# Optimization experiments

Hardware: AMD Instinct MI355X
Metric: run time of the kernel (lower is better)

The kernel has to match this reference:

```python
import math
import jax, jax.numpy as jnp
import numpy as np

NUM_PRE_NMS = 2000
NMS_THR = 0.7
MIN_SIZE = 16.0
LOG_MAX = math.log(1000.0 / 16)  # clamp on dh, dw as in the torch module

B, A, H, W = 8, 3, 200, 304
STRIDE = 4


def _make_anchors():
    # grid anchors, channel-last anchor ordering to match permute(0,2,3,1)
    sizes = np.array([32.0, 64.0, 128.0], dtype=np.float32)  # A sizes
    ys = (np.arange(H, dtype=np.float32) + 0.5) * STRIDE
    xs = (np.arange(W, dtype=np.float32) + 0.5) * STRIDE
    cy, cx = np.meshgrid(ys, xs, indexing="ij")  # [H,W]
    cx = cx[:, :, None]
    cy = cy[:, :, None]
    half = (sizes / 2.0)[None, None, :]  # [1,1,A]
    anc = np.stack([cx - half, cy - half, cx + half, cy + half], axis=-1)  # [H,W,A,4]
    anc = anc.reshape(-1, 4)  # [H*W*A, 4]
    anc = np.broadcast_to(anc[None], (B, anc.shape[0], 4)).copy()
    return jnp.asarray(anc)


def setup_inputs() -> dict:
    key = jax.random.key(0)
    k1, k2 = jax.random.split(key)
    cls_logits = jax.random.normal(k1, (B, A, H, W), dtype=jnp.float32)
    regs = jax.random.normal(k2, (B, 4 * A, H, W), dtype=jnp.float32) * 0.1
    anchors = _make_anchors()
    return {"cls_logits": cls_logits, "regs": regs, "anchors": anchors,
            "image_h": 800, "image_w": 1216}


def _box_iou(boxes):
    # boxes: [K,4] -> iou [K,K]
    x1, y1, x2, y2 = boxes[:, 0], boxes[:, 1], boxes[:, 2], boxes[:, 3]
    area = (x2 - x1) * (y2 - y1)
    ix1 = jnp.maximum(x1[:, None], x1[None, :])
    iy1 = jnp.maximum(y1[:, None], y1[None, :])
    ix2 = jnp.minimum(x2[:, None], x2[None, :])
    iy2 = jnp.minimum(y2[:, None], y2[None, :])
    iw = jnp.clip(ix2 - ix1, 0.0)
    ih = jnp.clip(iy2 - iy1, 0.0)
    inter = iw * ih
    union = area[:, None] + area[None, :] - inter
    return inter / jnp.maximum(union, 1e-6)


def _nms_one(boxes, valid):
    # boxes sorted by descending score; greedy suppression, fixed-size keep mask
    k = boxes.shape[0]
    iou = _box_iou(boxes)
    later = jnp.arange(k)

    def body(i, keep):
        sup = (iou[i] > NMS_THR) & keep[i] & (later > i)
        return keep & ~sup

    return jax.lax.fori_loop(0, k, body, valid)


def reference(cls_logits, regs, anchors, image_h, image_w):
    b = cls_logits.shape[0]
    # scores/regs in channel-last anchor order (matches permute(0,2,3,1))
    scores = jnp.transpose(cls_logits, (0, 2, 3, 1)).reshape(b, -1)       # [B,N]
    deltas = jnp.transpose(regs, (0, 2, 3, 1)).reshape(b, -1, 4)          # [B,N,4]
    n = scores.shape[1]
    k = min(NUM_PRE_NMS, n)

    top_scores, idx = jax.lax.top_k(scores, k)                            # [B,K]
    top_deltas = jnp.take_along_axis(deltas, idx[:, :, None], axis=1)     # [B,K,4]
    top_anchors = jnp.take_along_axis(anchors, idx[:, :, None], axis=1)   # [B,K,4]

    dx, dy = top_deltas[..., 0], top_deltas[..., 1]
    dh = jnp.minimum(top_deltas[..., 2], LOG_MAX)
    dw = jnp.minimum(top_deltas[..., 3], LOG_MAX)
    ah = top_anchors[..., 3] - top_anchors[..., 1]
    aw = top_anchors[..., 2] - top_anchors[..., 0]
    cx = aw / 2
    cy = ah / 2
    px = cx + dx * aw
    py = cy + dy * ah
    ph = jnp.exp(dh) * ah
    pw = jnp.exp(dw) * aw
    boxes = jnp.stack([px - pw / 2, py - ph / 2, px + pw / 2, py + ph / 2], axis=-1)  # [B,K,4]

    # size filter on clamped coords (as in _nms)
    w_img = jnp.float32(image_w)
    h_img = jnp.float32(image_h)
    bw = jnp.clip(boxes[..., 2], 0.0, w_img) - jnp.clip(boxes[..., 0], 0.0, w_img)
    bh = jnp.clip(boxes[..., 3], 0.0, h_img) - jnp.clip(boxes[..., 1], 0.0, h_img)
    valid = (bw >= MIN_SIZE) & (bh >= MIN_SIZE)

    keep = jax.vmap(_nms_one)(boxes, valid)                               # [B,K]
    out_boxes = boxes * keep[..., None].astype(boxes.dtype)
    return out_boxes, top_scores, keep
```

## Files before the change

kernel.cpp:

```cpp
#include <hip/hip_runtime.h>

#define HWSZ 60800
#define NA 3
#define NTOT 182400
#define KSEL 2000
#define CANDCAP 8192
#define SELCAP 4096
#define NBATCH 8
#define GSPLIT 128
#define LOG_MAX_F 4.135166556742356f

#define OFF_H1    0
#define OFF_CCNT  65536
#define OFF_SCNT  65568
#define ZR_BYTES  65600
#define OFF_SEL   65600
#define OFF_BOX   65728
#define OFF_VALID 321728
#define OFF_SUP   385728
#define OFF_CAND  385728
#define OFF_SELK  910016

__device__ __forceinline__ unsigned int xform(float f) {
    unsigned int b = __float_as_uint(f);
    return b ^ ((unsigned int)((int)b >> 31) | 0x80000000u);
}

__global__ __launch_bounds__(256) void k_hist1(const float* __restrict__ cls,
                                               unsigned int* __restrict__ hist1) {
    int b = blockIdx.y, part = blockIdx.x, tid = threadIdx.x;
    __shared__ unsigned int h[2048];
    for (int i = tid; i < 2048; i += 256) h[i] = 0u;
    __syncthreads();
    const float4* base4 = (const float4*)(cls + (size_t)b * NTOT);
    const int n4 = NTOT / 4;
    int per = (n4 + GSPLIT - 1) / GSPLIT;
    int lo = part * per, hi = lo + per;
    if (hi > n4) hi = n4;
    for (int i = lo + tid; i < hi; i += 256) {
        float4 v = base4[i];
        atomicAdd(&h[xform(v.x) >> 21], 1u);
        atomicAdd(&h[xform(v.y) >> 21], 1u);
        atomicAdd(&h[xform(v.z) >> 21], 1u);
        atomicAdd(&h[xform(v.w) >> 21], 1u);
    }
    __syncthreads();
    unsigned int* gh = hist1 + b * 2048;
    for (int i = tid; i < 2048; i += 256)
        if (h[i]) atomicAdd(&gh[i], h[i]);
}

__global__ __launch_bounds__(1024) void k_scan1(const unsigned int* __restrict__ hist1,
                                                uint4* __restrict__ selinfo) {
    int b = blockIdx.x, tid = threadIdx.x;
    __shared__ unsigned int sa[2048], sb[2048];
    const unsigned int* h = hist1 + b * 2048;
    sa[tid] = h[tid];
    sa[tid + 1024] = h[tid + 1024];
    unsigned int* src = sa; unsigned int* dst = sb;
    for (int d = 1; d < 2048; d <<= 1) {
        __syncthreads();
        dst[tid] = src[tid] + ((tid + d < 2048) ? src[tid + d] : 0u);
        int i2 = tid + 1024;
        dst[i2] = src[i2] + ((i2 + d < 2048) ? src[i2 + d] : 0u);
        unsigned int* t = src; src = dst; dst = t;
    }
    __syncthreads();
    #pragma unroll
    for (int k = 0; k < 2; ++k) {
        int i = tid + k * 1024;
        unsigned int c = src[i];
        unsigned int cn = (i < 2047) ? src[i + 1] : 0u;
        if (c >= KSEL && cn < KSEL)
            selinfo[b] = make_uint4((unsigned int)i, cn, KSEL - cn, 0u);
    }
}

__global__ __launch_bounds__(256) void k_gather(const float* __restrict__ cls,
                                                const uint4* __restrict__ selinfo,
                                                unsigned long long* __restrict__ cand,
                                                unsigned int* __restrict__ ccnt) {
    int b = blockIdx.y, part = blockIdx.x, tid = threadIdx.x;
    unsigned int bin = selinfo[b].x;
    __shared__ unsigned long long lbuf[1024];
    __shared__ unsigned int lcnt, gbase;
    if (tid == 0) lcnt = 0u;
    __syncthreads();
    const float4* base4 = (const float4*)(cls + (size_t)b * NTOT);
    const int n4 = NTOT / 4;
    int per = (n4 + GSPLIT - 1) / GSPLIT;
    int lo = part * per, hi = lo + per;
    if (hi > n4) hi = n4;
    for (int i = lo + tid; i < hi; i += 256) {
        float4 v = base4[i];
        float vals[4] = {v.x, v.y, v.z, v.w};
        int idx0 = i * 4;
        #pragma unroll
        for (int q = 0; q < 4; ++q) {
            unsigned int u = xform(vals[q]);
            if ((u >> 21) >= bin) {
                int idx = idx0 + q;
                int a = idx / HWSZ;
                int hw = idx - a * HWSZ;
                unsigned int n = (unsigned int)(hw * NA + a);
                unsigned int pos = atomicAdd(&lcnt, 1u);
                if (pos < 1024u)
                    lbuf[pos] = ((unsigned long long)u << 32) | (unsigned long long)(~n);
            }
        }
    }
    __syncthreads();
    if (tid == 0) {
        unsigned int c = lcnt < 1024u ? lcnt : 1024u;
        gbase = atomicAdd(&ccnt[b], c);
    }
    __syncthreads();
    unsigned int c = lcnt < 1024u ? lcnt : 1024u;
    unsigned int gb = gbase;
    for (unsigned int i = tid; i < c; i += 256) {
        unsigned int p = gb + i;
        if (p < CANDCAP) cand[(size_t)b * CANDCAP + p] = lbuf[i];
    }
}

__global__ __launch_bounds__(1024) void k_refine(const unsigned long long* __restrict__ cand,
                                                 const unsigned int* __restrict__ ccnt,
                                                 const uint4* __restrict__ selinfo,
                                                 unsigned long long* __restrict__ selk,
                                                 unsigned int* __restrict__ scnt) {
    int b = blockIdx.x;
    int tid = threadIdx.x;
    __shared__ unsigned int sa[2048], sb[2048];
    __shared__ unsigned int acnt, shT;
    uint4 si = selinfo[b];
    unsigned int bin = si.x, krem = si.z;
    unsigned int m = ccnt[b];
    if (m > CANDCAP) m = CANDCAP;
    const unsigned long long* cb = cand + (size_t)b * CANDCAP;

    sa[tid] = 0u; sa[tid + 1024] = 0u;
    if (tid == 0) acnt = 0u;
    __syncthreads();
    for (unsigned int i = tid; i < m; i += 1024) {
        unsigned int u = (unsigned int)(cb[i] >> 32);
        if ((u >> 21) == bin) atomicAdd(&sa[(u >> 10) & 2047u], 1u);
    }
    unsigned int* src = sa; unsigned int* dst = sb;
    for (int d = 1; d < 2048; d <<= 1) {
        __syncthreads();
        dst[tid] = src[tid] + ((tid + d < 2048) ? src[tid + d] : 0u);
        int i2 = tid + 1024;
        dst[i2] = src[i2] + ((i2 + d < 2048) ? src[i2 + d] : 0u);
        unsigned int* t = src; src = dst; dst = t;
    }
    __syncthreads();
    #pragma unroll
    for (int k = 0; k < 2; ++k) {
        int i = tid + k * 1024;
        unsigned int c = src[i];
        unsigned int cn = (i < 2047) ? src[i + 1] : 0u;
        if (c >= krem && cn < krem)
            shT = (bin << 21) | ((unsigned int)i << 10);
    }
    __syncthreads();
    unsigned int T = shT;

    int lane = tid & 63;
    unsigned long long lmask = (1ULL << lane) - 1ULL;
    unsigned int mr = (m + 1023u) & ~1023u;
    unsigned long long* sout = selk + (size_t)b * SELCAP;
    for (unsigned int i = tid; i < mr; i += 1024) {
        bool pred = false;
        unsigned long long key = 0ULL;
        if (i < m) {
            key = cb[i];
            pred = ((unsigned int)(key >> 32)) >= T;
        }
        unsigned long long mask = __ballot(pred);
        unsigned int cw = (unsigned int)__popcll(mask);
        unsigned int base = 0u;
        if (lane == 0 && cw) base = atomicAdd(&acnt, cw);
        base = __shfl(base, 0, 64);
        if (pred) {
            unsigned int pos = base + (unsigned int)__popcll(mask & lmask);
            if (pos < SELCAP) sout[pos] = key;
        }
    }
    __syncthreads();
    if (tid == 0) scnt[b] = (acnt < SELCAP) ? acnt : SELCAP;
}

__global__ __launch_bounds__(256) void k_rank_decode(
        const unsigned long long* __restrict__ selk,
        const unsigned int* __restrict__ scnt,
        const float* __restrict__ regs,
        const float* __restrict__ anchors,
        const int* __restrict__ img_h,
        const int* __restrict__ img_w,
        float* __restrict__ out_scores,
        float4* __restrict__ boxes_ws,
        unsigned int* __restrict__ valid_ws) {
    int b = blockIdx.y;
    int tid = threadIdx.x;
    unsigned int sc = scnt[b];
    if (sc > SELCAP) sc = SELCAP;
    unsigned int kbase = blockIdx.x * 64;
    if (kbase >= sc) return;
    int ki = tid & 63;
    int q = tid >> 6;
    int lane = tid & 63;
    const unsigned long long* sb_ = selk + (size_t)b * SELCAP;
    unsigned int r = kbase + (unsigned int)ki;
    unsigned long long mykey = (r < sc) ? sb_[r] : 0ULL;

    unsigned int qs = ((sc + 255u) >> 8) << 6;
    unsigned int lo = (unsigned int)q * qs;
    unsigned int hi = lo + qs;
    if (hi > sc) hi = sc;

    unsigned int cnt = 0u;
    for (unsigned int base = lo; base < hi; base += 64) {
        unsigned long long kj = 0ULL;
        if (base + (unsigned int)lane < hi) kj = sb_[base + lane];
        unsigned int klo = (unsigned int)kj;
        unsigned int khi = (unsigned int)(kj >> 32);
        #pragma unroll
        for (int t = 0; t < 64; ++t) {
            unsigned int lo_ = (unsigned int)__builtin_amdgcn_readlane((int)klo, t);
            unsigned int hi_ = (unsigned int)__builtin_amdgcn_readlane((int)khi, t);
            unsigned long long kt = ((unsigned long long)hi_ << 32) | (unsigned long long)lo_;
            cnt += (kt > mykey) ? 1u : 0u;
        }
    }
    __shared__ unsigned int cntsh[4][64];
    cntsh[q][ki] = cnt;
    __syncthreads();
    if (tid >= 64) return;
    unsigned int rank = cntsh[0][ki] + cntsh[1][ki] + cntsh[2][ki] + cntsh[3][ki];
    if (r >= sc || rank >= KSEL) return;

    int hv = img_h[0];
    int wv = img_w[0];
    float himg = (hv > 0 && hv < 100000) ? (float)hv : __int_as_float(hv);
    float wimg = (wv > 0 && wv < 100000) ? (float)wv : __int_as_float(wv);

    unsigned int u = (unsigned int)(mykey >> 32);
    unsigned int n = ~((unsigned int)mykey);
    unsigned int bits = (u & 0x80000000u) ? (u & 0x7FFFFFFFu) : ~u;
    float score = __uint_as_float(bits);
    int a = (int)(n % NA);
    int hw = (int)(n / NA);
    const float* rp = regs + ((size_t)b * (4 * NA) + 4 * a) * HWSZ + hw;
    float dx = rp[0 * HWSZ];
    float dy = rp[1 * HWSZ];
    float dh = rp[2 * HWSZ];
    float dw = rp[3 * HWSZ];
    const float* ap = anchors + ((size_t)b * NTOT + n) * 4;
    float ax1 = ap[0], ay1 = ap[1], ax2 = ap[2], ay2 = ap[3];
    float ahh = ay2 - ay1;
    float aww = ax2 - ax1;
    float cx = aww * 0.5f;
    float cy = ahh * 0.5f;
    float px = cx + dx * aww;
    float py = cy + dy * ahh;
    dh = fminf(dh, LOG_MAX_F);
    dw = fminf(dw, LOG_MAX_F);
    float ph = expf(dh) * ahh;
    float pw = expf(dw) * aww;
    float x1 = px - pw * 0.5f;
    float y1 = py - ph * 0.5f;
    float x2 = px + pw * 0.5f;
    float y2 = py + ph * 0.5f;
    float bwv = fminf(fmaxf(x2, 0.f), wimg) - fminf(fmaxf(x1, 0.f), wimg);
    float bhv = fminf(fmaxf(y2, 0.f), himg) - fminf(fmaxf(y1, 0.f), himg);
    unsigned int valid = (bwv >= 16.f && bhv >= 16.f) ? 1u : 0u;
    size_t o = (size_t)b * KSEL + rank;
    out_scores[o] = score;
    boxes_ws[o] = make_float4(x1, y1, x2, y2);
    valid_ws[o] = valid;
}

__global__ __launch_bounds__(256) void k_supmat(const float4* __restrict__ boxes_ws,
                                                unsigned long long* __restrict__ sup) {
    int ct = blockIdx.x;
    int rt = blockIdx.y;
    int b  = blockIdx.z;
    int tid = threadIdx.x;
    __shared__ float4 colbox[64];
    int j0 = ct * 64;
    if (tid < 64) {
        int jl = j0 + tid;
        colbox[tid] = (jl < KSEL) ? boxes_ws[(size_t)b * KSEL + jl]
                                  : make_float4(0.f, 0.f, 0.f, 0.f);
    }
    __syncthreads();
    int i = rt * 256 + tid;
    if (i >= KSEL) return;
    float4 bi = boxes_ws[(size_t)b * KSEL + i];
    float area_i = (bi.z - bi.x) * (bi.w - bi.y);
    unsigned long long word = 0ULL;
    #pragma unroll 8
    for (int jj = 0; jj < 64; ++jj) {
        int j = j0 + jj;
        float4 bj = colbox[jj];
        float area_j = (bj.z - bj.x) * (bj.w - bj.y);
        float ix1 = fmaxf(bi.x, bj.x);
        float iy1 = fmaxf(bi.y, bj.y);
        float ix2 = fminf(bi.z, bj.z);
        float iy2 = fminf(bi.w, bj.w);
        float iw = fmaxf(ix2 - ix1, 0.f);
        float ih = fmaxf(iy2 - iy1, 0.f);
        float inter = iw * ih;
        float uni = area_i + area_j - inter;
        float iou = inter / fmaxf(uni, 1e-6f);
        bool s = (j > i) && (j < KSEL) && (iou > 0.7f);
        if (s) word |= (1ULL << jj);
    }
    sup[((size_t)b * KSEL + i) * 32 + ct] = word;
}

#define LOAD_TILE(wnext, buf)                                                \
    {                                                                        \
        int gbase_ = (wnext) * 2048;                                         \
        _Pragma("unroll")                                                    \
        for (int k = 0; k < 8; ++k) {                                        \
            int e_ = tid + k * 256;                                          \
            int row_ = (wnext) * 64 + (e_ >> 5);                             \
            buf[k] = (row_ < KSEL) ? srow[gbase_ + e_] : 0ULL;               \
        }                                                                    \
    }

#define PROCESS_TILE(w, buf)                                                 \
    {                                                                        \
        if (myword == (w)) {                                                 \
            _Pragma("unroll")                                                \
            for (int k = 0; k < 8; ++k)                                      \
                diag[(tid >> 5) + k * 8] = buf[k];                           \
        }                                                                    \
        __syncthreads();      \
        unsigned long long dval_ = diag[lane];                               \
        unsigned long long nz_ = __ballot(dval_ != 0ULL);                    \
        unsigned int dlo_ = (unsigned int)dval_;                             \
        unsigned int dhi_ = (unsigned int)(dval_ >> 32);                     \
        unsigned long long pend_ =                                           \
            ((unsigned long long)accw[(w) * 2 + 1] << 32)                    \
            | (unsigned long long)accw[(w) * 2];                             \
        unsigned long long c64_ = kws[w] & ~pend_;                           \
        unsigned int clo_ = __builtin_amdgcn_readfirstlane((unsigned int)c64_);        \
        unsigned int chi_ = __builtin_amdgcn_readfirstlane((unsigned int)(c64_ >> 32));\
        unsigned long long cur_ = ((unsigned long long)chi_ << 32)           \
                                  | (unsigned long long)clo_;                \
        if (cur_) {                                                          \
             \
            unsigned long long rem_ = cur_ & nz_;                            \
            while (rem_) {                                                   \
                int bit_ = __builtin_ctzll(rem_);                            \
                unsigned int lo_ = (unsigned int)__builtin_amdgcn_readlane((int)dlo_, bit_); \
                unsigned int hi_ = (unsigned int)__builtin_amdgcn_readlane((int)dhi_, bit_); \
                unsigned long long d_ = ((unsigned long long)hi_ << 32)      \
                                        | (unsigned long long)lo_;           \
                cur_ &= ~d_;                                                 \
                rem_ = cur_ & nz_ & ~((2ULL << bit_) - 1ULL);                \
            }                                                                \
            if (tid == 0) fin[w] = cur_;                                     \
            unsigned long long v_ = 0ULL;                                    \
            _Pragma("unroll")                                                \
            for (int k = 0; k < 8; ++k) {                                    \
                int row_ = (tid >> 5) + k * 8;                               \
                if ((cur_ >> row_) & 1ULL) v_ |= buf[k];                     \
            }                                                                \
            v_ |= __shfl_xor(v_, 32, 64);                                    \
            if (lane < 32 && v_) {                                           \
                atomicOr(&accw[myword * 2], (unsigned int)v_);               \
                atomicOr(&accw[myword * 2 + 1], (unsigned int)(v_ >> 32));   \
            }                                                                \
        } else if (tid == 0) {                                               \
            fin[w] = 0ULL;                                                   \
        }                                                                    \
    }

__global__ __launch_bounds__(256) void k_nms_scan(const unsigned long long* __restrict__ sup,
                                                  const unsigned int* __restrict__ valid_ws,
                                                  const float4* __restrict__ boxes_ws,
                                                  float* __restrict__ out_boxes,
                                                  float* __restrict__ out_keep) {
    int b = blockIdx.x;
    int tid = threadIdx.x;
    int lane = tid & 63;
    int myword = tid & 31;
    __shared__ unsigned long long kws[32];
    __shared__ unsigned long long fin[32];
    __shared__ unsigned long long diag[64];
    __shared__ unsigned int accw[64];
    const unsigned long long* srow = sup + (size_t)b * KSEL * 32;

    if (tid < 32) {
        unsigned long long kw = 0ULL;
        const uint4* vv = (const uint4*)(valid_ws + (size_t)b * KSEL);
        #pragma unroll 4
        for (int q = 0; q < 16; ++q) {
            uint4 x = vv[tid * 16 + q];
            int base = q * 4;
            if (x.x) kw |= 1ULL << (base + 0);
            if (x.y) kw |= 1ULL << (base + 1);
            if (x.z) kw |= 1ULL << (base + 2);
            if (x.w) kw |= 1ULL << (base + 3);
        }
        if (tid == 31) kw &= 0xFFFFULL;
        kws[tid] = kw;
    }
    if (tid < 64) accw[tid] = 0u;

    unsigned long long A[8], B[8];
    LOAD_TILE(0, A);
    LOAD_TILE(1, B);

    for (int t = 0; t < 16; ++t) {
        int w = 2 * t;
        PROCESS_TILE(w, A);
        if (w + 2 < 32) LOAD_TILE(w + 2, A);
        PROCESS_TILE(w + 1, B);
        if (w + 3 < 32) LOAD_TILE(w + 3, B);
    }
    __syncthreads();

    for (int r = tid; r < KSEL; r += 256) {
        float kf = (float)((fin[r >> 6] >> (r & 63)) & 1ULL);
        size_t o = (size_t)b * KSEL + r;
        out_keep[o] = kf;
        float4 bx = boxes_ws[o];
        float* ob = out_boxes + o * 4;
        ob[0] = bx.x * kf;
        ob[1] = bx.y * kf;
        ob[2] = bx.z * kf;
        ob[3] = bx.w * kf;
    }
}

extern "C" void kernel_launch(void* const* d_in, const int* in_sizes, int n_in,
                              void* d_out, int out_size, void* d_ws, size_t ws_size,
                              hipStream_t stream) {
    const float* cls     = (const float*)d_in[0];
    const float* regs    = (const float*)d_in[1];
    const float* anchors = (const float*)d_in[2];
    const int*   img_h   = (const int*)d_in[3];
    const int*   img_w   = (const int*)d_in[4];

    float* out = (float*)d_out;
    float* out_boxes  = out;
    float* out_scores = out + 64000;
    float* out_keep   = out + 80000;

    char* ws = (char*)d_ws;
    unsigned int* hist1      = (unsigned int*)(ws + OFF_H1);
    unsigned int* ccnt       = (unsigned int*)(ws + OFF_CCNT);
    unsigned int* scnt       = (unsigned int*)(ws + OFF_SCNT);
    uint4* selinfo           = (uint4*)(ws + OFF_SEL);
    float4* boxes_ws         = (float4*)(ws + OFF_BOX);
    unsigned int* valid_ws   = (unsigned int*)(ws + OFF_VALID);
    unsigned long long* sup  = (unsigned long long*)(ws + OFF_SUP);
    unsigned long long* cand = (unsigned long long*)(ws + OFF_CAND);
    unsigned long long* selk = (unsigned long long*)(ws + OFF_SELK);

    hipMemsetAsync(ws, 0, ZR_BYTES, stream);
    k_hist1<<<dim3(GSPLIT, NBATCH), 256, 0, stream>>>(cls, hist1);
    k_scan1<<<NBATCH, 1024, 0, stream>>>(hist1, selinfo);
    k_gather<<<dim3(GSPLIT, NBATCH), 256, 0, stream>>>(cls, selinfo, cand, ccnt);
    k_refine<<<NBATCH, 1024, 0, stream>>>(cand, ccnt, selinfo, selk, scnt);
    k_rank_decode<<<dim3(SELCAP / 64, NBATCH), 256, 0, stream>>>(selk, scnt, regs, anchors,
                                                                 img_h, img_w, out_scores,
                                                                 boxes_ws, valid_ws);
    k_supmat<<<dim3(32, 8, NBATCH), 256, 0, stream>>>(boxes_ws, sup);
    k_nms_scan<<<NBATCH, 256, 0, stream>>>(sup, valid_ws, boxes_ws, out_boxes, out_keep);
}
```

Measured before the change: 200.7 us.

## Fuse histogram scan into last block, drop refine pass, skip lower-triangle suppression tiles

The histogram kernel now runs the prefix scan itself: an atomic done-counter picks the last block per batch, which removes a separate launch. The refine kernel is deleted, so rank_decode ranks every gathered candidate directly (up to CANDCAP), with its grid widened to match. The suppression-matrix kernel skips tiles that lie entirely below the diagonal, NMS accumulation ignores words that are already final, and box output is written as float4. These changes cut launches and redundant work, but ranking now covers a larger candidate set and its cost grows quadratically with it.

After: 244.6 us. +21.9%, slower.

```diff
diff --git a/kernel.cpp b/kernel.cpp
--- a/kernel.cpp
+++ b/kernel.cpp
@@ -5,29 +5,29 @@
 #define NTOT 182400
 #define KSEL 2000
 #define CANDCAP 8192
-#define SELCAP 4096
 #define NBATCH 8
 #define GSPLIT 128
 #define LOG_MAX_F 4.135166556742356f
 
 #define OFF_H1    0
 #define OFF_CCNT  65536
-#define OFF_SCNT  65568
+#define OFF_DONE  65568
 #define ZR_BYTES  65600
 #define OFF_SEL   65600
 #define OFF_BOX   65728
 #define OFF_VALID 321728
 #define OFF_SUP   385728
 #define OFF_CAND  385728
-#define OFF_SELK  910016
 
 __device__ __forceinline__ unsigned int xform(float f) {
     unsigned int b = __float_as_uint(f);
     return b ^ ((unsigned int)((int)b >> 31) | 0x80000000u);
 }
 
-__global__ __launch_bounds__(256) void k_hist1(const float* __restrict__ cls,
-                                               unsigned int* __restrict__ hist1) {
+__global__ __launch_bounds__(256) void k_hist_scan(const float* __restrict__ cls,
+                                                   unsigned int* __restrict__ hist1,
+                                                   unsigned int* __restrict__ done,
+                                                   uint4* __restrict__ selinfo) {
     int b = blockIdx.y, part = blockIdx.x, tid = threadIdx.x;
     __shared__ unsigned int h[2048];
     for (int i = tid; i < 2048; i += 256) h[i] = 0u;
@@ -48,27 +48,38 @@
     unsigned int* gh = hist1 + b * 2048;
     for (int i = tid; i < 2048; i += 256)
         if (h[i]) atomicAdd(&gh[i], h[i]);
-}
-
-__global__ __launch_bounds__(1024) void k_scan1(const unsigned int* __restrict__ hist1,
-                                                uint4* __restrict__ selinfo) {
-    int b = blockIdx.x, tid = threadIdx.x;
+
+    __shared__ unsigned int slast;
+    __syncthreads();
+    if (tid == 0) {
+        __threadfence();
+        unsigned int old = __hip_atomic_fetch_add(&done[b], 1u, __ATOMIC_ACQ_REL,
+                                                  __HIP_MEMORY_SCOPE_AGENT);
+        slast = (old == GSPLIT - 1) ? 1u : 0u;
+    }
+    __syncthreads();
+    if (!slast) return;
+
     __shared__ unsigned int sa[2048], sb[2048];
-    const unsigned int* h = hist1 + b * 2048;
-    sa[tid] = h[tid];
-    sa[tid + 1024] = h[tid + 1024];
+    #pragma unroll
+    for (int k = 0; k < 8; ++k) {
+        int i = tid + k * 256;
+        sa[i] = __hip_atomic_load(&gh[i], __ATOMIC_RELAXED, __HIP_MEMORY_SCOPE_AGENT);
+    }
     unsigned int* src = sa; unsigned int* dst = sb;
     for (int d = 1; d < 2048; d <<= 1) {
         __syncthreads();
-        dst[tid] = src[tid] + ((tid + d < 2048) ? src[tid + d] : 0u);
-        int i2 = tid + 1024;
-        dst[i2] = src[i2] + ((i2 + d < 2048) ? src[i2 + d] : 0u);
+        #pragma unroll
+        for (int k = 0; k < 8; ++k) {
+            int i = tid + k * 256;
+            dst[i] = src[i] + ((i + d < 2048) ? src[i + d] : 0u);
+        }
         unsigned int* t = src; src = dst; dst = t;
     }
     __syncthreads();
     #pragma unroll
-    for (int k = 0; k < 2; ++k) {
-        int i = tid + k * 1024;
+    for (int k = 0; k < 8; ++k) {
+        int i = tid + k * 256;
         unsigned int c = src[i];
         unsigned int cn = (i < 2047) ? src[i + 1] : 0u;
         if (c >= KSEL && cn < KSEL)
@@ -123,76 +134,9 @@
     }
 }
 
-__global__ __launch_bounds__(1024) void k_refine(const unsigned long long* __restrict__ cand,
-                                                 const unsigned int* __restrict__ ccnt,
-                                                 const uint4* __restrict__ selinfo,
-                                                 unsigned long long* __restrict__ selk,
-                                                 unsigned int* __restrict__ scnt) {
-    int b = blockIdx.x;
-    int tid = threadIdx.x;
-    __shared__ unsigned int sa[2048], sb[2048];
-    __shared__ unsigned int acnt, shT;
-    uint4 si = selinfo[b];
-    unsigned int bin = si.x, krem = si.z;
-    unsigned int m = ccnt[b];
-    if (m > CANDCAP) m = CANDCAP;
-    const unsigned long long* cb = cand + (size_t)b * CANDCAP;
-
-    sa[tid] = 0u; sa[tid + 1024] = 0u;
-    if (tid == 0) acnt = 0u;
-    __syncthreads();
-    for (unsigned int i = tid; i < m; i += 1024) {
-        unsigned int u = (unsigned int)(cb[i] >> 32);
-        if ((u >> 21) == bin) atomicAdd(&sa[(u >> 10) & 2047u], 1u);
-    }
-    unsigned int* src = sa; unsigned int* dst = sb;
-    for (int d = 1; d < 2048; d <<= 1) {
-        __syncthreads();
-        dst[tid] = src[tid] + ((tid + d < 2048) ? src[tid + d] : 0u);
-        int i2 = tid + 1024;
-        dst[i2] = src[i2] + ((i2 + d < 2048) ? src[i2 + d] : 0u);
-        unsigned int* t = src; src = dst; dst = t;
-    }
-    __syncthreads();
-    #pragma unroll
-    for (int k = 0; k < 2; ++k) {
-        int i = tid + k * 1024;
-        unsigned int c = src[i];
-        unsigned int cn = (i < 2047) ? src[i + 1] : 0u;
-        if (c >= krem && cn < krem)
-            shT = (bin << 21) | ((unsigned int)i << 10);
-    }
-    __syncthreads();
-    unsigned int T = shT;
-
-    int lane = tid & 63;
-    unsigned long long lmask = (1ULL << lane) - 1ULL;
-    unsigned int mr = (m + 1023u) & ~1023u;
-    unsigned long long* sout = selk + (size_t)b * SELCAP;
-    for (unsigned int i = tid; i < mr; i += 1024) {
-        bool pred = false;
-        unsigned long long key = 0ULL;
-        if (i < m) {
-            key = cb[i];
-            pred = ((unsigned int)(key >> 32)) >= T;
-        }
-        unsigned long long mask = __ballot(pred);
-        unsigned int cw = (unsigned int)__popcll(mask);
-        unsigned int base = 0u;
-        if (lane == 0 && cw) base = atomicAdd(&acnt, cw);
-        base = __shfl(base, 0, 64);
-        if (pred) {
-            unsigned int pos = base + (unsigned int)__popcll(mask & lmask);
-            if (pos < SELCAP) sout[pos] = key;
-        }
-    }
-    __syncthreads();
-    if (tid == 0) scnt[b] = (acnt < SELCAP) ? acnt : SELCAP;
-}
-
 __global__ __launch_bounds__(256) void k_rank_decode(
-        const unsigned long long* __restrict__ selk,
-        const unsigned int* __restrict__ scnt,
+        const unsigned long long* __restrict__ cand,
+        const unsigned int* __restrict__ ccnt,
         const float* __restrict__ regs,
         const float* __restrict__ anchors,
         const int* __restrict__ img_h,
@@ -202,14 +146,14 @@
         unsigned int* __restrict__ valid_ws) {
     int b = blockIdx.y;
     int tid = threadIdx.x;
-    unsigned int sc = scnt[b];
-    if (sc > SELCAP) sc = SELCAP;
+    unsigned int sc = ccnt[b];
+    if (sc > CANDCAP) sc = CANDCAP;
     unsigned int kbase = blockIdx.x * 64;
     if (kbase >= sc) return;
     int ki = tid & 63;
     int q = tid >> 6;
     int lane = tid & 63;
-    const unsigned long long* sb_ = selk + (size_t)b * SELCAP;
+    const unsigned long long* sb_ = cand + (size_t)b * CANDCAP;
     unsigned int r = kbase + (unsigned int)ki;
     unsigned long long mykey = (r < sc) ? sb_[r] : 0ULL;
 
@@ -285,6 +229,7 @@
     int ct = blockIdx.x;
     int rt = blockIdx.y;
     int b  = blockIdx.z;
+    if (ct * 64 + 63 < rt * 256) return;
     int tid = threadIdx.x;
     __shared__ float4 colbox[64];
     int j0 = ct * 64;
@@ -370,7 +315,7 @@
                 if ((cur_ >> row_) & 1ULL) v_ |= buf[k];                     \
             }                                                                \
             v_ |= __shfl_xor(v_, 32, 64);                                    \
-            if (lane < 32 && v_) {                                           \
+            if (lane < 32 && myword > (w) && v_) {                           \
                 atomicOr(&accw[myword * 2], (unsigned int)v_);               \
                 atomicOr(&accw[myword * 2 + 1], (unsigned int)(v_ >> 32));   \
             }                                                                \
@@ -424,16 +369,13 @@
     }
     __syncthreads();
 
+    float4* ob4 = (float4*)out_boxes;
     for (int r = tid; r < KSEL; r += 256) {
         float kf = (float)((fin[r >> 6] >> (r & 63)) & 1ULL);
         size_t o = (size_t)b * KSEL + r;
         out_keep[o] = kf;
         float4 bx = boxes_ws[o];
-        float* ob = out_boxes + o * 4;
-        ob[0] = bx.x * kf;
-        ob[1] = bx.y * kf;
-        ob[2] = bx.z * kf;
-        ob[3] = bx.w * kf;
+        ob4[o] = make_float4(bx.x * kf, bx.y * kf, bx.z * kf, bx.w * kf);
     }
 }
 
@@ -454,22 +396,19 @@
     char* ws = (char*)d_ws;
     unsigned int* hist1      = (unsigned int*)(ws + OFF_H1);
     unsigned int* ccnt       = (unsigned int*)(ws + OFF_CCNT);
-    unsigned int* scnt       = (unsigned int*)(ws + OFF_SCNT);
+    unsigned int* done       = (unsigned int*)(ws + OFF_DONE);
     uint4* selinfo           = (uint4*)(ws + OFF_SEL);
     float4* boxes_ws         = (float4*)(ws + OFF_BOX);
     unsigned int* valid_ws   = (unsigned int*)(ws + OFF_VALID);
     unsigned long long* sup  = (unsigned long long*)(ws + OFF_SUP);
     unsigned long long* cand = (unsigned long long*)(ws + OFF_CAND);
-    unsigned long long* selk = (unsigned long long*)(ws + OFF_SELK);
 
     hipMemsetAsync(ws, 0, ZR_BYTES, stream);
-    k_hist1<<<dim3(GSPLIT, NBATCH), 256, 0, stream>>>(cls, hist1);
-    k_scan1<<<NBATCH, 1024, 0, stream>>>(hist1, selinfo);
+    k_hist_scan<<<dim3(GSPLIT, NBATCH), 256, 0, stream>>>(cls, hist1, done, selinfo);
     k_gather<<<dim3(GSPLIT, NBATCH), 256, 0, stream>>>(cls, selinfo, cand, ccnt);
-    k_refine<<<NBATCH, 1024, 0, stream>>>(cand, ccnt, selinfo, selk, scnt);
-    k_rank_decode<<<dim3(SELCAP / 64, NBATCH), 256, 0, stream>>>(selk, scnt, regs, anchors,
-                                                                 img_h, img_w, out_scores,
-                                                                 boxes_ws, valid_ws);
+    k_rank_decode<<<dim3(CANDCAP / 64, NBATCH), 256, 0, stream>>>(cand, ccnt, regs, anchors,
+                                                                  img_h, img_w, out_scores,
+                                                                  boxes_ws, valid_ws);
     k_supmat<<<dim3(32, 8, NBATCH), 256, 0, stream>>>(boxes_ws, sup);
     k_nms_scan<<<NBATCH, 256, 0, stream>>>(sup, valid_ws, boxes_ws, out_boxes, out_keep);
 }
```
